# Kernel optimization log

Hardware: AMD Instinct MI355X
Metric: run time of the kernel (lower is better)

## Reference

```python
import jax, jax.numpy as jnp
import numpy as np

N = 50000   # nodes
E = 600000  # edges / hyperedge incidences
D = 128     # node_in_dim
H = 128     # hidden_dim
TAU = 0.5
ALPHA = 0.5
LAM = 0.5

_PARAM_SHAPES = [('Wq0', (1, H)), ('bq0', (H,)), ('W0', (D, H)), ('b0', (H,)),
                 ('Whq0', (1, H)), ('bhq0', (H,)), ('Wh0', (D, H)), ('bh0', (H,)),
                 ('Wf0', (H, H)), ('bf0', (H,)), ('Wfh0', (H, H)), ('bfh0', (H,)),
                 ('aq0', (H,)), ('a0', (H,)), ('ahq0', (H,)), ('ah0', (H,)),
                 ('aq_', (H,)), ('a_', (H,)), ('ahq_', (H,)), ('ah_', (H,)),
                 ('Wlq', (1, H)), ('blq', (H,)), ('Wlf', (D, H)), ('blf', (H,)),
                 ('Wm1', (H, H)), ('bm1', (H,)), ('Wm2', (H, H)), ('bm2', (H,))]


def setup_inputs() -> dict:
    key = jax.random.key(0)
    ks = jax.random.split(key, 8 + len(_PARAM_SHAPES))
    inp = {}
    inp['feats'] = jax.random.normal(ks[0], (N, D), dtype=jnp.float32)
    inp['edge_index'] = jax.random.randint(ks[1], (2, E), 0, N).astype(jnp.int32)
    inp['edge_index_aug'] = jax.random.randint(ks[2], (2, E), 0, N).astype(jnp.int32)
    inp['pos'] = jax.random.randint(ks[3], (100,), 1, N).astype(jnp.int32)
    inp['q'] = 0
    for i, (nm, sh) in enumerate(_PARAM_SHAPES):
        inp[nm] = jax.random.normal(ks[4 + i], sh, dtype=jnp.float32) * 0.05
    return inp


def _forward(feats, Wq0, bq0, W0, b0, Whq0, bhq0, Wh0, bh0, Wf0, bf0, Wfh0, bfh0,
             aq0, a0, ahq0, ah0, aq_, a_, ahq_, ah_, Wlq, blq, Wlf, blf,
             Wm1, bm1, Wm2, bm2, edge_index, edge_index_aug, q, pos):
    # ---- GCNConv (PyG default: add self-loops + symmetric normalization) ----
    sl = jnp.arange(N, dtype=edge_index.dtype)
    src = jnp.concatenate([edge_index[0], sl])
    dst = jnp.concatenate([edge_index[1], sl])
    deg = jax.ops.segment_sum(jnp.ones(src.shape[0], jnp.float32), dst, num_segments=N)
    dinv = jax.lax.rsqrt(deg)  # deg >= 1 thanks to self-loops
    enorm = dinv[src] * dinv[dst]

    def gcn(x, W, b):
        xw = x @ W
        return jax.ops.segment_sum(xw[src] * enorm[:, None], dst, num_segments=N) + b

    # ---- HypergraphConv (PyG, no attention): X' = D^-1 H B^-1 H^T X W ----
    node = edge_index_aug[0]
    he = edge_index_aug[1]
    Be = jax.ops.segment_sum(jnp.ones((E,), jnp.float32), he, num_segments=N)
    Dn = jax.ops.segment_sum(jnp.ones((E,), jnp.float32), node, num_segments=N)
    Binv = jnp.where(Be > 0, 1.0 / Be, 0.0)
    Dninv = jnp.where(Dn > 0, 1.0 / Dn, 0.0)

    def hg(x, W, b):
        xw = x @ W
        me = jax.ops.segment_sum(xw[node], he, num_segments=N) * Binv[:, None]
        return jax.ops.segment_sum(me[he], node, num_segments=N) * Dninv[:, None] + b

    # ---- attention-weighted fusion of two views (softmax over 2 logits) ----
    def fuse(a, b, wa, wb):
        att = jax.nn.softmax(jnp.stack([a @ wa, b @ wb], axis=1), axis=1)  # [N,2]
        return att[:, 0:1] * a + att[:, 1:2] * b

    querys = jnp.zeros((N, 1), jnp.float32).at[q].set(1.0)
    hq = jax.nn.relu(gcn(querys, Wq0, bq0))
    h = jax.nn.relu(gcn(feats, W0, b0))
    hf = fuse(hq, h, aq0, a0)
    h_augq = jax.nn.relu(hg(querys, Whq0, bhq0))
    h_aug = jax.nn.relu(hg(feats, Wh0, bh0))
    h_augf = fuse(h_augq, h_aug, ahq0, ah0)
    querys2 = querys @ Wlq + blq
    feats2 = feats @ Wlf + blf
    hf_ = fuse(querys2, feats2, aq_, a_)
    hf = jax.nn.relu(hf + gcn(hf_, Wf0, bf0))
    hfh_ = fuse(querys2, feats2, ahq_, ah_)
    h_augf = jax.nn.relu(h_augf + hg(hfh_, Wfh0, bfh0))

    def mlp(x):
        return jax.nn.relu(x @ Wm1 + bm1) @ Wm2 + bm2

    z = mlp(hf)
    z_aug = mlp(h_augf)

    # ---- Contra loss ----
    def expcos(v, M):
        num = M @ v
        den = jnp.maximum(jnp.linalg.norm(M, axis=1) * jnp.linalg.norm(v), 1e-8)
        return jnp.exp(num / den / TAU)

    sim1 = expcos(z[q], z)
    sim_aug1 = expcos(z_aug[q], z_aug)
    sim2 = expcos(z[q], z_aug)
    sim_aug2 = expcos(z_aug[q], z)
    mask = jnp.zeros((N,), bool).at[pos].set(True).at[q].set(False)
    nmask = jnp.sum(mask).astype(jnp.float32)

    def nlm(s):  # mean over positives of -log(s_i / sum(s))
        r = jnp.log(jnp.sum(s)) - jnp.log(s)
        return jnp.sum(jnp.where(mask, r, 0.0)) / nmask

    loss_intra = 0.5 * (nlm(sim1) + nlm(sim_aug1))
    loss_inter = 0.5 * (nlm(sim2) + nlm(sim_aug2))
    z_unsup = jnp.log(jnp.sum(sim2)) - jnp.log(sim2[q])
    z_aug_unsup = jnp.log(jnp.sum(sim_aug2)) - jnp.log(sim_aug2[q])
    loss_unsup = 0.5 * z_unsup + 0.5 * z_aug_unsup
    return loss_intra + ALPHA * loss_inter + LAM * loss_unsup


def reference(feats, Wq0, bq0, W0, b0, Whq0, bhq0, Wh0, bh0, Wf0, bf0, Wfh0, bfh0,
              aq0, a0, ahq0, ah0, aq_, a_, ahq_, ah_, Wlq, blq, Wlf, blf,
              Wm1, bm1, Wm2, bm2, edge_index, edge_index_aug, q, pos):
    return _forward(feats, Wq0, bq0, W0, b0, Whq0, bhq0, Wh0, bh0, Wf0, bf0, Wfh0, bfh0,
                    aq0, a0, ahq0, ah0, aq_, a_, ahq_, ah_, Wlq, blq, Wlf, blf,
                    Wm1, bm1, Wm2, bm2, edge_index, edge_index_aug, q, pos)
```

## Files before the change

kernel.cpp:

```cpp
#include <hip/hip_runtime.h>

#define NN 50000
#define EE 600000
#define HH 128
#define TAU_INV 2.0f
#define PSZ 6250
#define CAP 48
#define SSTR 64

typedef __attribute__((ext_vector_type(8))) short short8;
typedef __attribute__((ext_vector_type(4))) float f32x4;
typedef __attribute__((ext_vector_type(2))) float floatx2;

__device__ __forceinline__ float wsum64(float v) {
#pragma unroll
  for (int m = 32; m >= 1; m >>= 1) v += __shfl_xor(v, m, 64);
  return v;
}
__device__ __forceinline__ unsigned short f2bf(float f) {
  unsigned u = __builtin_bit_cast(unsigned, f);
  u = u + 0x7FFFu + ((u >> 16) & 1u);
  return (unsigned short)(u >> 16);
}
__device__ __forceinline__ float bf2f(unsigned short h) {
  unsigned u = ((unsigned)h) << 16;
  return __builtin_bit_cast(float, u);
}
__device__ __forceinline__ unsigned char fp8_enc1(float v) {
  int p = __builtin_amdgcn_cvt_pk_fp8_f32(v, v, 0, false);
  return (unsigned char)(p & 0xFF);
}
__device__ __forceinline__ void fp8x8_dec(uint2 v, float* f) {
  floatx2 a = __builtin_amdgcn_cvt_pk_f32_fp8(v.x, false);
  floatx2 b = __builtin_amdgcn_cvt_pk_f32_fp8(v.x, true);
  floatx2 c = __builtin_amdgcn_cvt_pk_f32_fp8(v.y, false);
  floatx2 d = __builtin_amdgcn_cvt_pk_f32_fp8(v.y, true);
  f[0] = a.x; f[1] = a.y; f[2] = b.x; f[3] = b.y;
  f[4] = c.x; f[5] = c.y; f[6] = d.x; f[7] = d.y;
}
__device__ __forceinline__ uint2 fp8x8_enc(const float* f) {
  int w0 = __builtin_amdgcn_cvt_pk_fp8_f32(f[0], f[1], 0, false);
  w0 = __builtin_amdgcn_cvt_pk_fp8_f32(f[2], f[3], w0, true);
  int w1 = __builtin_amdgcn_cvt_pk_fp8_f32(f[4], f[5], 0, false);
  w1 = __builtin_amdgcn_cvt_pk_fp8_f32(f[6], f[7], w1, true);
  return make_uint2((unsigned)w0, (unsigned)w1);
}

#define LDSW 136


__device__ __forceinline__ void fill_body(const int* __restrict__ ei,
                                          const int* __restrict__ ea,
                                          const int* __restrict__ qp, int* __restrict__ cursor,
                                          unsigned short* __restrict__ slotsA,
                                          unsigned short* __restrict__ slotsB,
                                          unsigned short* __restrict__ slotsC,
                                          float* __restrict__ cntq, int blk, int nblk) {
  const int p = blk & 7;
  const int lo = p * PSZ, hi = lo + PSZ;
  const int q = *qp;
  const int stride = (nblk >> 3) * 256;
  for (int e = (blk >> 3) * 256 + threadIdx.x; e < EE; e += stride) {
    int src = ei[e], dst = ei[EE + e];
    if (dst >= lo && dst < hi) {
      int idx = atomicAdd(&cursor[dst], 1);
      if (idx < CAP) slotsA[dst * SSTR + idx] = (unsigned short)src;
    }
    int node = ea[e], he = ea[EE + e];
    if (he >= lo && he < hi) {
      int idx = atomicAdd(&cursor[NN + he], 1);
      if (idx < CAP) slotsB[he * SSTR + idx] = (unsigned short)node;
      if (node == q) atomicAdd(&cntq[he], 1.0f);
    }
    if (node >= lo && node < hi) {
      int idx = atomicAdd(&cursor[2 * NN + node], 1);
      if (idx < CAP) slotsC[node * SSTR + idx] = (unsigned short)he;
    }
  }
}

__device__ __forceinline__ void pack_body(const float* __restrict__ W0,
                                          const float* __restrict__ Wh0,
                                          const float* __restrict__ Wlf,
                                          const float* __restrict__ Wf0,
                                          const float* __restrict__ Wfh0,
                                          const float* __restrict__ Wm1,
                                          const float* __restrict__ Wm2,
                                          unsigned short* __restrict__ out, int blk) {
  int tid = blk * 256 + threadIdx.x;
  if (tid >= 7 * 2048) return;
  int mat = tid >> 11, r = tid & 2047;
  int s = r >> 9, c = (r >> 6) & 7, lane = r & 63;
  const float* W = (mat == 0) ? W0 : (mat == 1) ? Wh0 : (mat == 2) ? Wlf
                 : (mat == 3) ? Wf0 : (mat == 4) ? Wfh0 : (mat == 5) ? Wm1 : Wm2;
  int k0 = 32 * s + (lane >> 4) * 8;
  int n = 16 * c + (lane & 15);
  unsigned short* o = out + (size_t)tid * 8;
#pragma unroll
  for (int j = 0; j < 8; ++j) o[j] = f2bf(W[(k0 + j) * 128 + n]);
}

__device__ __forceinline__ void derive_body(const int* __restrict__ cursor,
                                            float* __restrict__ dinv, float* __restrict__ Binv,
                                            float* __restrict__ Dninv,
                                            const int* __restrict__ pos,
                                            const int* __restrict__ qp,
                                            int* __restrict__ maskI, int blk) {
  int i = blk * 256 + threadIdx.x;
  if (i < NN) {
    dinv[i] = rsqrtf((float)(cursor[i] + 1));
    int b = cursor[NN + i];
    Binv[i] = (b > 0) ? 1.0f / (float)b : 0.0f;
    int d = cursor[2 * NN + i];
    Dninv[i] = (d > 0) ? 1.0f / (float)d : 0.0f;
  }
  if (blk == 0) {
    int t = threadIdx.x;
    if (t < 100) maskI[pos[t]] = 1;
    __syncthreads();
    if (t == 0) maskI[*qp] = 0;
  }
}

__device__ __forceinline__ void shq_body(const int* __restrict__ ei, const int* __restrict__ ea,
                                         const int* __restrict__ qp,
                                         const int* __restrict__ cursor,
                                         const float* __restrict__ cntq,
                                         float* __restrict__ s_hq, float* __restrict__ s_hgq,
                                         int blk) {
  int e = blk * 256 + threadIdx.x;
  if (e >= EE) return;
  int q = *qp;
  int src = ei[e];
  if (src == q) {
    int dst = ei[EE + e];
    float dq = rsqrtf((float)(cursor[q] + 1));
    atomicAdd(&s_hq[dst], dq * rsqrtf((float)(cursor[dst] + 1)));
  }
  int he = ea[EE + e];
  float cq = cntq[he];
  if (cq != 0.0f) {
    int node = ea[e];
    atomicAdd(&s_hgq[node], cq / (float)cursor[NN + he]);
  }
  if (e == 0) atomicAdd(&s_hq[q], 1.0f / (float)(cursor[q] + 1));
}

template <bool BIAS, int OM>
__device__ __forceinline__ void gemm_core_rt(const unsigned short* As, const short8* Wp,
                                             const float* bias, void* outv, int r0, int nrows,
                                             int tid, int relu) {
  const int wave = tid >> 6, lane = tid & 63;
  const int quad = lane >> 4, l15 = lane & 15;
  const int rw = r0 + wave * 16;
  f32x4 acc[8];
#pragma unroll
  for (int c = 0; c < 8; ++c) acc[c] = (f32x4){0.f, 0.f, 0.f, 0.f};
#pragma unroll
  for (int s = 0; s < 4; ++s) {
    short8 a = *(const short8*)&As[(wave * 16 + l15) * LDSW + s * 32 + quad * 8];
#pragma unroll
    for (int c = 0; c < 8; ++c) {
      short8 b = Wp[(s * 8 + c) * 64 + lane];
      acc[c] = __builtin_amdgcn_mfma_f32_16x16x32_bf16(a, b, acc[c], 0, 0, 0);
    }
  }
#pragma unroll
  for (int c = 0; c < 8; ++c) {
    int col = c * 16 + l15;
    float bv = BIAS ? bias[col] : 0.f;
#pragma unroll
    for (int r = 0; r < 4; ++r) {
      int grow = rw + quad * 4 + r;
      if (grow < nrows) {
        float v = acc[c][r] + bv;
        if (relu) v = fmaxf(v, 0.f);
        if (OM == 2)
          ((unsigned char*)outv)[(size_t)grow * 256 + col] = fp8_enc1(v);
        else
          ((unsigned short*)outv)[(size_t)grow * 128 + col] = f2bf(v);
      }
    }
  }
}

__device__ __forceinline__ void stage_bf16(const unsigned short* A, unsigned short* As,
                                           int r0, int nrows, int tid) {
#pragma unroll
  for (int t = 0; t < 4; ++t) {
    int v = t * 256 + tid;
    int row = v >> 4, cc = v & 15;
    int gr = r0 + row;
    uint4 val = make_uint4(0, 0, 0, 0);
    if (gr < nrows) val = ((const uint4*)A)[(size_t)gr * 16 + cc];
    *(uint4*)&As[row * LDSW + cc * 8] = val;
  }
}

__device__ __forceinline__ void gemm3_body(unsigned short* As, const float* __restrict__ A,
                                           const short8* __restrict__ Wp,
                                           const float* __restrict__ bias2,
                                           unsigned char* __restrict__ p1,
                                           unsigned char* __restrict__ p2,
                                           unsigned short* __restrict__ out2, int nrows,
                                           int blk) {
  const int tid = threadIdx.x;
  const int r0 = blk * 64;
#pragma unroll
  for (int t = 0; t < 8; ++t) {
    int v = t * 256 + tid;
    int row = v >> 5, c4 = v & 31;
    int gr = r0 + row;
    float4 val = make_float4(0.f, 0.f, 0.f, 0.f);
    if (gr < nrows) val = ((const float4*)A)[(size_t)gr * 32 + c4];
    ushort4 o;
    o.x = f2bf(val.x); o.y = f2bf(val.y); o.z = f2bf(val.z); o.w = f2bf(val.w);
    *(ushort4*)&As[row * LDSW + c4 * 4] = o;
  }
  __syncthreads();
  const int wave = tid >> 6, lane = tid & 63;
  const int quad = lane >> 4, l15 = lane & 15;
  const int rw = r0 + wave * 16;
  f32x4 acc[3][8];
#pragma unroll
  for (int m = 0; m < 3; ++m)
#pragma unroll
    for (int c = 0; c < 8; ++c) acc[m][c] = (f32x4){0.f, 0.f, 0.f, 0.f};
#pragma unroll
  for (int s = 0; s < 4; ++s) {
    short8 a = *(const short8*)&As[(wave * 16 + l15) * LDSW + s * 32 + quad * 8];
#pragma unroll
    for (int m = 0; m < 3; ++m)
#pragma unroll
      for (int c = 0; c < 8; ++c) {
        short8 b = Wp[(size_t)m * 2048 + (s * 8 + c) * 64 + lane];
        acc[m][c] = __builtin_amdgcn_mfma_f32_16x16x32_bf16(a, b, acc[m][c], 0, 0, 0);
      }
  }
#pragma unroll
  for (int c = 0; c < 8; ++c) {
    int col = c * 16 + l15;
    float bv = bias2[col];
#pragma unroll
    for (int r = 0; r < 4; ++r) {
      int grow = rw + quad * 4 + r;
      if (grow < nrows) {
        p1[(size_t)grow * 256 + col] = fp8_enc1(acc[0][c][r]);
        p2[(size_t)grow * 256 + col] = fp8_enc1(acc[1][c][r]);
        out2[(size_t)grow * 128 + col] = f2bf(acc[2][c][r] + bv);
      }
    }
  }
}

template <int MODE, bool OUTFP8>
__device__ __forceinline__ void gpair_body(const uint2* __restrict__ xp,
                                           unsigned short* __restrict__ y1,
                                           unsigned short* __restrict__ y2,
                                           uint2* __restrict__ yp,
                                           const int* __restrict__ cnt,
                                           const unsigned short* __restrict__ slots,
                                           const float* __restrict__ wv, int blk) {
  int node = blk * 8 + (threadIdx.x >> 5);
  if (node >= NN) return;
  int l = threadIdx.x & 31;
  int st = node * SSTR;
  int n = min(cnt[node], CAP);
  float acc[8];
#pragma unroll
  for (int i = 0; i < 8; ++i) acc[i] = 0.f;
  int p = 0;
  for (; p + 4 <= n; p += 4) {
    ushort4 s4 = *(const ushort4*)&slots[st + p];
    uint2 v0 = xp[(size_t)s4.x * 32 + l];
    uint2 v1 = xp[(size_t)s4.y * 32 + l];
    uint2 v2 = xp[(size_t)s4.z * 32 + l];
    uint2 v3 = xp[(size_t)s4.w * 32 + l];
    float f[8];
    if (MODE == 0) {
      float w0 = wv[s4.x], w1 = wv[s4.y], w2 = wv[s4.z], w3 = wv[s4.w];
      fp8x8_dec(v0, f);
#pragma unroll
      for (int i = 0; i < 8; ++i) acc[i] = fmaf(w0, f[i], acc[i]);
      fp8x8_dec(v1, f);
#pragma unroll
      for (int i = 0; i < 8; ++i) acc[i] = fmaf(w1, f[i], acc[i]);
      fp8x8_dec(v2, f);
#pragma unroll
      for (int i = 0; i < 8; ++i) acc[i] = fmaf(w2, f[i], acc[i]);
      fp8x8_dec(v3, f);
#pragma unroll
      for (int i = 0; i < 8; ++i) acc[i] = fmaf(w3, f[i], acc[i]);
    } else {
      fp8x8_dec(v0, f);
#pragma unroll
      for (int i = 0; i < 8; ++i) acc[i] += f[i];
      fp8x8_dec(v1, f);
#pragma unroll
      for (int i = 0; i < 8; ++i) acc[i] += f[i];
      fp8x8_dec(v2, f);
#pragma unroll
      for (int i = 0; i < 8; ++i) acc[i] += f[i];
      fp8x8_dec(v3, f);
#pragma unroll
      for (int i = 0; i < 8; ++i) acc[i] += f[i];
    }
  }
  for (; p < n; ++p) {
    int s = slots[st + p];
    uint2 v = xp[(size_t)s * 32 + l];
    float f[8];
    fp8x8_dec(v, f);
    if (MODE == 0) {
      float w = wv[s];
#pragma unroll
      for (int i = 0; i < 8; ++i) acc[i] = fmaf(w, f[i], acc[i]);
    } else {
#pragma unroll
      for (int i = 0; i < 8; ++i) acc[i] += f[i];
    }
  }
  float sc = wv[node];
  if (MODE == 0) {
    uint2 v = xp[(size_t)node * 32 + l];
    float f[8];
    fp8x8_dec(v, f);
#pragma unroll
    for (int i = 0; i < 8; ++i) acc[i] = sc * fmaf(sc, f[i], acc[i]);
  } else {
#pragma unroll
    for (int i = 0; i < 8; ++i) acc[i] *= sc;
  }
  if (OUTFP8) {
    yp[(size_t)node * 32 + l] = fp8x8_enc(acc);
  } else {
    unsigned short* y = (l < 16) ? y1 : y2;
    int cg = l & 15;
    uint4 o;
    o.x = ((unsigned)f2bf(acc[1]) << 16) | f2bf(acc[0]);
    o.y = ((unsigned)f2bf(acc[3]) << 16) | f2bf(acc[2]);
    o.z = ((unsigned)f2bf(acc[5]) << 16) | f2bf(acc[4]);
    o.w = ((unsigned)f2bf(acc[7]) << 16) | f2bf(acc[6]);
    *(uint4*)&y[(size_t)node * 128 + cg * 8] = o;
  }
}

__device__ __forceinline__ void fuse_add_body(const unsigned short* __restrict__ g,
                                              const unsigned short* __restrict__ gr,
                                              const float* __restrict__ svec,
                                              const float* __restrict__ dscale,
                                              const float* __restrict__ Wq,
                                              const float* __restrict__ bq,
                                              const float* __restrict__ bm,
                                              const float* __restrict__ aq,
                                              const float* __restrict__ am,
                                              const float* __restrict__ bres,
                                              unsigned short* __restrict__ out, int blk) {
  int row = blk * 4 + (threadIdx.x >> 6);
  if (row >= NN) return;
  int lane = threadIdx.x & 63;
  int c0 = lane, c1 = lane + 64;
  float s = svec[row];
  if (dscale) s *= dscale[row];
  float hq0 = fmaxf(fmaf(s, Wq[c0], bq[c0]), 0.f);
  float hq1 = fmaxf(fmaf(s, Wq[c1], bq[c1]), 0.f);
  float h0 = fmaxf(bf2f(g[(size_t)row * 128 + c0]) + bm[c0], 0.f);
  float h1 = fmaxf(bf2f(g[(size_t)row * 128 + c1]) + bm[c1], 0.f);
  float dq = wsum64(hq0 * aq[c0] + hq1 * aq[c1]);
  float dm = wsum64(h0 * am[c0] + h1 * am[c1]);
  float mx = fmaxf(dq, dm);
  float e0 = expf(dq - mx), e1 = expf(dm - mx);
  float w0 = e0 / (e0 + e1), w1 = 1.f - w0;
  float r0 = fmaxf(w0 * hq0 + w1 * h0 + bf2f(gr[(size_t)row * 128 + c0]) + bres[c0], 0.f);
  float r1 = fmaxf(w0 * hq1 + w1 * h1 + bf2f(gr[(size_t)row * 128 + c1]) + bres[c1], 0.f);
  out[(size_t)row * 128 + c0] = f2bf(r0);
  out[(size_t)row * 128 + c1] = f2bf(r1);
}


__global__ __launch_bounds__(256) void fill_pack_k(
    const int* ei, const int* ea, const int* qp, int* cursor, unsigned short* slotsA,
    unsigned short* slotsB, unsigned short* slotsC, float* cntq, int fb, const float* W0,
    const float* Wh0, const float* Wlf, const float* Wf0, const float* Wfh0, const float* Wm1,
    const float* Wm2, unsigned short* Wpack) {
  int b = blockIdx.x;
  if (b < fb)
    fill_body(ei, ea, qp, cursor, slotsA, slotsB, slotsC, cntq, b, fb);
  else
    pack_body(W0, Wh0, Wlf, Wf0, Wfh0, Wm1, Wm2, Wpack, b - fb);
}

__global__ __launch_bounds__(256) void g3ds_k(
    const float* A, const short8* Wp, const float* bias2, unsigned char* p1, unsigned char* p2,
    unsigned short* out2, int gmb, const int* cursor, float* dinv, float* Binv, float* Dninv,
    const int* pos, const int* qp, int* maskI, const int* ei, const int* ea, const float* cntq,
    float* s_hq, float* s_hgq, int nb) {
  __shared__ unsigned short As[64 * LDSW];
  int b = blockIdx.x;
  if (b < gmb) {
    gemm3_body(As, A, Wp, bias2, p1, p2, out2, NN, b);
    return;
  }
  b -= gmb;
  if (b < nb) {
    derive_body(cursor, dinv, Binv, Dninv, pos, qp, maskI, b);
    return;
  }
  shq_body(ei, ea, qp, cursor, cntq, s_hq, s_hgq, b - nb);
}

__global__ void fuse2_k(const unsigned short* __restrict__ f2, const int* __restrict__ qp,
                        const float* __restrict__ Wlq, const float* __restrict__ blq,
                        const float* __restrict__ aq1, const float* __restrict__ a1,
                        const float* __restrict__ aq2, const float* __restrict__ a2,
                        unsigned short* __restrict__ out1, unsigned short* __restrict__ out2) {
  int row = blockIdx.x * 4 + (threadIdx.x >> 6);
  if (row >= NN) return;
  int lane = threadIdx.x & 63;
  int c0 = lane, c1 = lane + 64;
  int q = *qp;
  float q20 = blq[c0] + ((row == q) ? Wlq[c0] : 0.f);
  float q21 = blq[c1] + ((row == q) ? Wlq[c1] : 0.f);
  float f0 = bf2f(f2[(size_t)row * 128 + c0]);
  float f1 = bf2f(f2[(size_t)row * 128 + c1]);
  float dq1 = wsum64(q20 * aq1[c0] + q21 * aq1[c1]);
  float df1 = wsum64(f0 * a1[c0] + f1 * a1[c1]);
  float dq2 = wsum64(q20 * aq2[c0] + q21 * aq2[c1]);
  float df2 = wsum64(f0 * a2[c0] + f1 * a2[c1]);
  {
    float mx = fmaxf(dq1, df1);
    float e0 = expf(dq1 - mx), e1 = expf(df1 - mx);
    float w0 = e0 / (e0 + e1), w1 = 1.f - w0;
    out1[(size_t)row * 128 + c0] = f2bf(w0 * q20 + w1 * f0);
    out1[(size_t)row * 128 + c1] = f2bf(w0 * q21 + w1 * f1);
  }
  {
    float mx = fmaxf(dq2, df2);
    float e0 = expf(dq2 - mx), e1 = expf(df2 - mx);
    float w0 = e0 / (e0 + e1), w1 = 1.f - w0;
    out2[(size_t)row * 128 + c0] = f2bf(w0 * q20 + w1 * f0);
    out2[(size_t)row * 128 + c1] = f2bf(w0 * q21 + w1 * f1);
  }
}

__global__ __launch_bounds__(256) void gemm2f8_k(const unsigned short* A0,
                                                 const unsigned short* A1, const short8* Wp0,
                                                 const short8* Wp1, unsigned char* o0,
                                                 unsigned char* o1, int nblk) {
  __shared__ unsigned short As[64 * LDSW];
  int b = blockIdx.x;
  const unsigned short* A = A0;
  const short8* Wp = Wp0;
  unsigned char* o = o0;
  if (b >= nblk) {
    b -= nblk; A = A1; Wp = Wp1; o = o1;
  }
  stage_bf16(A, As, b * 64, NN, threadIdx.x);
  __syncthreads();
  gemm_core_rt<false, 2>(As, Wp, nullptr, o, b * 64, NN, threadIdx.x, 0);
}

__global__ void dgather12_k(const uint2* __restrict__ xp1, unsigned short* __restrict__ y1a,
                            unsigned short* __restrict__ y1b, const uint2* __restrict__ xp2,
                            uint2* __restrict__ yp3, const int* __restrict__ cursor,
                            const unsigned short* __restrict__ slotsA,
                            const unsigned short* __restrict__ slotsB,
                            const float* __restrict__ dinv, const float* __restrict__ Binv,
                            int nblk) {
  int b = blockIdx.x;
  if (b < nblk)
    gpair_body<0, false>(xp1, y1a, y1b, nullptr, cursor, slotsA, dinv, b);
  else
    gpair_body<1, true>(xp2, nullptr, nullptr, yp3, cursor + NN, slotsB, Binv, b - nblk);
}

__global__ void g3fa_k(const uint2* xp, unsigned short* y1, unsigned short* y2,
                       const int* cursor, const unsigned short* slotsC, const float* Dninv,
                       int gtb, const unsigned short* g, const unsigned short* gr,
                       const float* svec, const float* Wq, const float* bq, const float* bm,
                       const float* aq, const float* am, const float* bres,
                       unsigned short* out) {
  int b = blockIdx.x;
  if (b < gtb)
    gpair_body<1, false>(xp, y1, y2, nullptr, cursor + 2 * NN, slotsC, Dninv, b);
  else
    fuse_add_body(g, gr, svec, nullptr, Wq, bq, bm, aq, am, bres, out, b - gtb);
}

__global__ __launch_bounds__(256) void fagemm_k(
    const unsigned short* g, const unsigned short* gr, const float* svec, const float* dscale,
    const float* Wq, const float* bq, const float* bm, const float* aq, const float* am,
    const float* bres, unsigned short* out, int rb, const unsigned short* A, const short8* Wp,
    const float* bias, unsigned short* o, int relu) {
  __shared__ unsigned short As[64 * LDSW];
  int b = blockIdx.x;
  if (b < rb) {
    fuse_add_body(g, gr, svec, dscale, Wq, bq, bm, aq, am, bres, out, b);
    return;
  }
  b -= rb;
  stage_bf16(A, As, b * 64, NN, threadIdx.x);
  __syncthreads();
  gemm_core_rt<true, 1>(As, Wp, bias, o, b * 64, NN, threadIdx.x, relu);
}

__global__ __launch_bounds__(256) void gemm2x_k(const unsigned short* A0,
                                                const unsigned short* A1, const short8* Wp0,
                                                const short8* Wp1, const float* b0,
                                                const float* b1, unsigned short* o0,
                                                unsigned short* o1, int nblk, int relu0,
                                                int relu1) {
  __shared__ unsigned short As[64 * LDSW];
  int b = blockIdx.x;
  const unsigned short* A = A0;
  const short8* Wp = Wp0;
  const float* bias = b0;
  unsigned short* o = o0;
  int relu = relu0;
  if (b >= nblk) {
    b -= nblk; A = A1; Wp = Wp1; bias = b1; o = o1; relu = relu1;
  }
  stage_bf16(A, As, b * 64, NN, threadIdx.x);
  __syncthreads();
  gemm_core_rt<true, 1>(As, Wp, bias, o, b * 64, NN, threadIdx.x, relu);
}

__global__ void sim_k(const unsigned short* __restrict__ z,
                      const unsigned short* __restrict__ za, const int* __restrict__ qp,
                      float4* __restrict__ simbuf, float* __restrict__ scal_out) {
  int row = blockIdx.x * 4 + (threadIdx.x >> 6);
  if (row >= NN) return;
  int lane = threadIdx.x & 63;
  int c0 = lane, c1 = lane + 64;
  int q = *qp;
  float zi0 = bf2f(z[(size_t)row * 128 + c0]), zi1 = bf2f(z[(size_t)row * 128 + c1]);
  float zai0 = bf2f(za[(size_t)row * 128 + c0]), zai1 = bf2f(za[(size_t)row * 128 + c1]);
  float zq0 = bf2f(z[(size_t)q * 128 + c0]), zq1 = bf2f(z[(size_t)q * 128 + c1]);
  float zaq0 = bf2f(za[(size_t)q * 128 + c0]), zaq1 = bf2f(za[(size_t)q * 128 + c1]);
  float nzi = wsum64(zi0 * zi0 + zi1 * zi1);
  float nzai = wsum64(zai0 * zai0 + zai1 * zai1);
  float nzq = wsum64(zq0 * zq0 + zq1 * zq1);
  float nzaq = wsum64(zaq0 * zaq0 + zaq1 * zaq1);
  float d1 = wsum64(zi0 * zq0 + zi1 * zq1);
  float d2 = wsum64(zai0 * zaq0 + zai1 * zaq1);
  float d3 = wsum64(zai0 * zq0 + zai1 * zq1);
  float d4 = wsum64(zi0 * zaq0 + zi1 * zaq1);
  if (lane == 0) {
    float ni = sqrtf(nzi), nai = sqrtf(nzai);
    float nq = sqrtf(nzq), naq = sqrtf(nzaq);
    float c1_ = d1 / fmaxf(ni * nq, 1e-8f) * TAU_INV;
    float ca1 = d2 / fmaxf(nai * naq, 1e-8f) * TAU_INV;
    float c2_ = d3 / fmaxf(nai * nq, 1e-8f) * TAU_INV;
    float ca2 = d4 / fmaxf(ni * naq, 1e-8f) * TAU_INV;
    simbuf[row] = make_float4(c1_, ca1, c2_, ca2);
    if (row == q) {
      scal_out[9] = c2_;
      scal_out[10] = ca2;
    }
  }
}

__global__ __launch_bounds__(256) void reduce_sim_k(const float4* __restrict__ simbuf,
                                                    const int* __restrict__ maskI,
                                                    float* __restrict__ scal) {
  float acc[9];
#pragma unroll
  for (int i = 0; i < 9; ++i) acc[i] = 0.f;
  for (int row = blockIdx.x * 256 + threadIdx.x; row < NN; row += gridDim.x * 256) {
    float4 v = simbuf[row];
    acc[0] += expf(v.x);
    acc[1] += expf(v.y);
    acc[2] += expf(v.z);
    acc[3] += expf(v.w);
    if (maskI[row]) {
      acc[4] += v.x; acc[5] += v.y; acc[6] += v.z; acc[7] += v.w;
      acc[8] += 1.0f;
    }
  }
  __shared__ float s[9][4];
  int lane = threadIdx.x & 63, wv = threadIdx.x >> 6;
#pragma unroll
  for (int i = 0; i < 9; ++i) {
    float r = wsum64(acc[i]);
    if (lane == 0) s[i][wv] = r;
  }
  __syncthreads();
  if (threadIdx.x < 9) {
    float r = s[threadIdx.x][0] + s[threadIdx.x][1] + s[threadIdx.x][2] + s[threadIdx.x][3];
    atomicAdd(&scal[threadIdx.x], r);
  }
}

__global__ void final_k(const float* __restrict__ scal, float* __restrict__ out) {
  if (threadIdx.x != 0 || blockIdx.x != 0) return;
  float S1 = scal[0], Sa1 = scal[1], S2 = scal[2], Sa2 = scal[3];
  float L1 = scal[4], La1 = scal[5], L2 = scal[6], La2 = scal[7];
  float NM = scal[8], Q2 = scal[9], Qa2 = scal[10];
  float intra = 0.5f * ((logf(S1) - L1 / NM) + (logf(Sa1) - La1 / NM));
  float inter = 0.5f * ((logf(S2) - L2 / NM) + (logf(Sa2) - La2 / NM));
  float unsup = 0.5f * (logf(S2) - Q2) + 0.5f * (logf(Sa2) - Qa2);
  out[0] = intra + 0.5f * inter + 0.5f * unsup;
}

extern "C" void kernel_launch(void* const* d_in, const int* in_sizes, int n_in,
                              void* d_out, int out_size, void* d_ws, size_t ws_size,
                              hipStream_t stream) {
  const float* feats = (const float*)d_in[0];
  const int* ei = (const int*)d_in[1];
  const int* ea = (const int*)d_in[2];
  const int* pos = (const int*)d_in[3];
  const int* qp = (const int*)d_in[4];
  const float* Wq0 = (const float*)d_in[5];
  const float* bq0 = (const float*)d_in[6];
  const float* W0 = (const float*)d_in[7];
  const float* b0 = (const float*)d_in[8];
  const float* Whq0 = (const float*)d_in[9];
  const float* bhq0 = (const float*)d_in[10];
  const float* Wh0 = (const float*)d_in[11];
  const float* bh0 = (const float*)d_in[12];
  const float* Wf0 = (const float*)d_in[13];
  const float* bf0 = (const float*)d_in[14];
  const float* Wfh0 = (const float*)d_in[15];
  const float* bfh0 = (const float*)d_in[16];
  const float* aq0 = (const float*)d_in[17];
  const float* a0 = (const float*)d_in[18];
  const float* ahq0 = (const float*)d_in[19];
  const float* ah0 = (const float*)d_in[20];
  const float* aq_ = (const float*)d_in[21];
  const float* a_ = (const float*)d_in[22];
  const float* ahq_ = (const float*)d_in[23];
  const float* ah_ = (const float*)d_in[24];
  const float* Wlq = (const float*)d_in[25];
  const float* blq = (const float*)d_in[26];
  const float* Wlf = (const float*)d_in[27];
  const float* blf = (const float*)d_in[28];
  const float* Wm1 = (const float*)d_in[29];
  const float* bm1 = (const float*)d_in[30];
  const float* Wm2 = (const float*)d_in[31];
  const float* bm2 = (const float*)d_in[32];

  char* ws = (char*)d_ws;
  size_t off = 0;
  auto take = [&](size_t bytes) -> void* {
    void* p = ws + off;
    off = (off + bytes + 255) & ~(size_t)255;
    return p;
  };
  int* cursor3 = (int*)take(3 * NN * 4);
  int* maskI = (int*)take(NN * 4);
  float* s_hq = (float*)take(NN * 4);
  float* cntq = (float*)take(NN * 4);
  float* s_hgq = (float*)take(NN * 4);
  float* scal = (float*)take(64 * 4);
  size_t zero_end = off;
  unsigned short* slotsA = (unsigned short*)take((size_t)NN * SSTR * 2);
  unsigned short* slotsB = (unsigned short*)take((size_t)NN * SSTR * 2);
  unsigned short* slotsC = (unsigned short*)take((size_t)NN * SSTR * 2);
  float* dinv = (float*)take(NN * 4);
  float* Binv = (float*)take(NN * 4);
  float* Dninv = (float*)take(NN * 4);
  float4* simbuf = (float4*)take((size_t)NN * 16);
  unsigned short* Wpack = (unsigned short*)take((size_t)7 * 16384 * 2);
  const size_t BFSZ = (size_t)NN * HH * 2;
  unsigned short* B0 = (unsigned short*)take(BFSZ);
  unsigned short* B1 = (unsigned short*)take(BFSZ);
  unsigned short* B2 = (unsigned short*)take(BFSZ);
  unsigned short* B3 = (unsigned short*)take(BFSZ);
  unsigned short* B4 = (unsigned short*)take(BFSZ);
  unsigned short* B5 = (unsigned short*)take(BFSZ);
  unsigned short* B6 = (unsigned short*)take(BFSZ);
  unsigned char* P1 = (unsigned char*)take((size_t)NN * 256);
  unsigned char* P2 = (unsigned char*)take((size_t)NN * 256);
  unsigned char* P3 = (unsigned char*)take((size_t)NN * 256);

  const int NB = (NN + 255) / 256;
  const int EB = (EE + 255) / 256;
  const int GMB = (NN + 63) / 64;
  const int GTB = (NN + 7) / 8;
  const int RB = (NN + 3) / 4;
  const int FB = 4096;
  const int PB = 56;
  const short8* Wp = (const short8*)Wpack;

  hipMemsetAsync(d_ws, 0, zero_end, stream);
  fill_pack_k<<<FB + PB, 256, 0, stream>>>(ei, ea, qp, cursor3, slotsA, slotsB, slotsC, cntq,
                                           FB, W0, Wh0, Wlf, Wf0, Wfh0, Wm1, Wm2, Wpack);
  g3ds_k<<<GMB + NB + EB, 256, 0, stream>>>(feats, Wp, blf, P1, P2, B6, GMB, cursor3, dinv,
                                            Binv, Dninv, pos, qp, maskI, ei, ea, cntq, s_hq,
                                            s_hgq, NB);
  fuse2_k<<<RB, 256, 0, stream>>>(B6, qp, Wlq, blq, aq_, a_, ahq_, ah_, B3, B4);
  gemm2f8_k<<<2 * GMB, 256, 0, stream>>>(B3, B4, Wp + (size_t)3 * 2048, Wp + (size_t)4 * 2048,
                                         P1 + 128, P2 + 128, GMB);
  dgather12_k<<<2 * GTB, 256, 0, stream>>>((const uint2*)P1, B0, B1, (const uint2*)P2,
                                           (uint2*)P3, cursor3, slotsA, slotsB, dinv, Binv,
                                           GTB);
  g3fa_k<<<GTB + RB, 256, 0, stream>>>((const uint2*)P3, B2, B5, cursor3, slotsC, Dninv, GTB,
                                       B0, B1, s_hq, Wq0, bq0, b0, aq0, a0, bf0, B3);
  fagemm_k<<<RB + GMB, 256, 0, stream>>>(B2, B5, s_hgq, Dninv, Whq0, bhq0, bh0, ahq0, ah0,
                                         bfh0, B4, RB, B3, Wp + (size_t)5 * 2048, bm1, B0, 1);
  gemm2x_k<<<2 * GMB, 256, 0, stream>>>(B4, B0, Wp + (size_t)5 * 2048, Wp + (size_t)6 * 2048,
                                        bm1, bm2, B1, B2, GMB, 1, 0);
  gemm2x_k<<<GMB, 256, 0, stream>>>(B1, B1, Wp + (size_t)6 * 2048, Wp + (size_t)6 * 2048, bm2,
                                    bm2, B5, B5, GMB, 0, 0);
  sim_k<<<RB, 256, 0, stream>>>(B2, B5, qp, simbuf, scal);
  reduce_sim_k<<<64, 256, 0, stream>>>(simbuf, maskI, scal);
  final_k<<<1, 64, 0, stream>>>(scal, (float*)d_out);
}
```

Baseline: 477.2 us.

## Regroup early kernels to overlap fill with GEMM, unroll gather by eight

Weight packing moves into its own small kernel so the first GEMM can share a launch with the edge-fill pass. The degree derivation, query-scalar and fuse2 steps merge into a single launch, which removes one kernel boundary. The gather loop now loads eight slot indices with one 16-byte read and issues eight independent row loads, and the slot stride is reduced to match the capacity. Costs are higher register pressure in the gather and a mixed-work launch whose GEMM blocks compete with atomic-heavy fill blocks.

```diff
diff --git a/kernel.cpp b/kernel.cpp
--- a/kernel.cpp
+++ b/kernel.cpp
@@ -6,7 +6,7 @@
 #define TAU_INV 2.0f
 #define PSZ 6250
 #define CAP 48
-#define SSTR 64
+#define SSTR 48
 
 typedef __attribute__((ext_vector_type(8))) short short8;
 typedef __attribute__((ext_vector_type(4))) float f32x4;
@@ -79,27 +79,6 @@
   }
 }
 
-__device__ __forceinline__ void pack_body(const float* __restrict__ W0,
-                                          const float* __restrict__ Wh0,
-                                          const float* __restrict__ Wlf,
-                                          const float* __restrict__ Wf0,
-                                          const float* __restrict__ Wfh0,
-                                          const float* __restrict__ Wm1,
-                                          const float* __restrict__ Wm2,
-                                          unsigned short* __restrict__ out, int blk) {
-  int tid = blk * 256 + threadIdx.x;
-  if (tid >= 7 * 2048) return;
-  int mat = tid >> 11, r = tid & 2047;
-  int s = r >> 9, c = (r >> 6) & 7, lane = r & 63;
-  const float* W = (mat == 0) ? W0 : (mat == 1) ? Wh0 : (mat == 2) ? Wlf
-                 : (mat == 3) ? Wf0 : (mat == 4) ? Wfh0 : (mat == 5) ? Wm1 : Wm2;
-  int k0 = 32 * s + (lane >> 4) * 8;
-  int n = 16 * c + (lane & 15);
-  unsigned short* o = out + (size_t)tid * 8;
-#pragma unroll
-  for (int j = 0; j < 8; ++j) o[j] = f2bf(W[(k0 + j) * 128 + n]);
-}
-
 __device__ __forceinline__ void derive_body(const int* __restrict__ cursor,
                                             float* __restrict__ dinv, float* __restrict__ Binv,
                                             float* __restrict__ Dninv,
@@ -270,15 +249,22 @@
 #pragma unroll
   for (int i = 0; i < 8; ++i) acc[i] = 0.f;
   int p = 0;
-  for (; p + 4 <= n; p += 4) {
-    ushort4 s4 = *(const ushort4*)&slots[st + p];
-    uint2 v0 = xp[(size_t)s4.x * 32 + l];
-    uint2 v1 = xp[(size_t)s4.y * 32 + l];
-    uint2 v2 = xp[(size_t)s4.z * 32 + l];
-    uint2 v3 = xp[(size_t)s4.w * 32 + l];
+  for (; p + 8 <= n; p += 8) {
+    uint4 sl = *(const uint4*)&slots[st + p];
+    int i0 = sl.x & 0xFFFF, i1 = sl.x >> 16, i2 = sl.y & 0xFFFF, i3 = sl.y >> 16;
+    int i4 = sl.z & 0xFFFF, i5 = sl.z >> 16, i6 = sl.w & 0xFFFF, i7 = sl.w >> 16;
+    uint2 v0 = xp[(size_t)i0 * 32 + l];
+    uint2 v1 = xp[(size_t)i1 * 32 + l];
+    uint2 v2 = xp[(size_t)i2 * 32 + l];
+    uint2 v3 = xp[(size_t)i3 * 32 + l];
+    uint2 v4 = xp[(size_t)i4 * 32 + l];
+    uint2 v5 = xp[(size_t)i5 * 32 + l];
+    uint2 v6 = xp[(size_t)i6 * 32 + l];
+    uint2 v7 = xp[(size_t)i7 * 32 + l];
     float f[8];
     if (MODE == 0) {
-      float w0 = wv[s4.x], w1 = wv[s4.y], w2 = wv[s4.z], w3 = wv[s4.w];
+      float w0 = wv[i0], w1 = wv[i1], w2 = wv[i2], w3 = wv[i3];
+      float w4 = wv[i4], w5 = wv[i5], w6 = wv[i6], w7 = wv[i7];
       fp8x8_dec(v0, f);
 #pragma unroll
       for (int i = 0; i < 8; ++i) acc[i] = fmaf(w0, f[i], acc[i]);
@@ -291,6 +277,18 @@
       fp8x8_dec(v3, f);
 #pragma unroll
       for (int i = 0; i < 8; ++i) acc[i] = fmaf(w3, f[i], acc[i]);
+      fp8x8_dec(v4, f);
+#pragma unroll
+      for (int i = 0; i < 8; ++i) acc[i] = fmaf(w4, f[i], acc[i]);
+      fp8x8_dec(v5, f);
+#pragma unroll
+      for (int i = 0; i < 8; ++i) acc[i] = fmaf(w5, f[i], acc[i]);
+      fp8x8_dec(v6, f);
+#pragma unroll
+      for (int i = 0; i < 8; ++i) acc[i] = fmaf(w6, f[i], acc[i]);
+      fp8x8_dec(v7, f);
+#pragma unroll
+      for (int i = 0; i < 8; ++i) acc[i] = fmaf(w7, f[i], acc[i]);
     } else {
       fp8x8_dec(v0, f);
 #pragma unroll
@@ -302,6 +300,18 @@
 #pragma unroll
       for (int i = 0; i < 8; ++i) acc[i] += f[i];
       fp8x8_dec(v3, f);
+#pragma unroll
+      for (int i = 0; i < 8; ++i) acc[i] += f[i];
+      fp8x8_dec(v4, f);
+#pragma unroll
+      for (int i = 0; i < 8; ++i) acc[i] += f[i];
+      fp8x8_dec(v5, f);
+#pragma unroll
+      for (int i = 0; i < 8; ++i) acc[i] += f[i];
+      fp8x8_dec(v6, f);
+#pragma unroll
+      for (int i = 0; i < 8; ++i) acc[i] += f[i];
+      fp8x8_dec(v7, f);
 #pragma unroll
       for (int i = 0; i < 8; ++i) acc[i] += f[i];
     }
@@ -377,44 +387,17 @@
   out[(size_t)row * 128 + c1] = f2bf(r1);
 }
 
-
-__global__ __launch_bounds__(256) void fill_pack_k(
-    const int* ei, const int* ea, const int* qp, int* cursor, unsigned short* slotsA,
-    unsigned short* slotsB, unsigned short* slotsC, float* cntq, int fb, const float* W0,
-    const float* Wh0, const float* Wlf, const float* Wf0, const float* Wfh0, const float* Wm1,
-    const float* Wm2, unsigned short* Wpack) {
-  int b = blockIdx.x;
-  if (b < fb)
-    fill_body(ei, ea, qp, cursor, slotsA, slotsB, slotsC, cntq, b, fb);
-  else
-    pack_body(W0, Wh0, Wlf, Wf0, Wfh0, Wm1, Wm2, Wpack, b - fb);
-}
-
-__global__ __launch_bounds__(256) void g3ds_k(
-    const float* A, const short8* Wp, const float* bias2, unsigned char* p1, unsigned char* p2,
-    unsigned short* out2, int gmb, const int* cursor, float* dinv, float* Binv, float* Dninv,
-    const int* pos, const int* qp, int* maskI, const int* ei, const int* ea, const float* cntq,
-    float* s_hq, float* s_hgq, int nb) {
-  __shared__ unsigned short As[64 * LDSW];
-  int b = blockIdx.x;
-  if (b < gmb) {
-    gemm3_body(As, A, Wp, bias2, p1, p2, out2, NN, b);
-    return;
-  }
-  b -= gmb;
-  if (b < nb) {
-    derive_body(cursor, dinv, Binv, Dninv, pos, qp, maskI, b);
-    return;
-  }
-  shq_body(ei, ea, qp, cursor, cntq, s_hq, s_hgq, b - nb);
-}
-
-__global__ void fuse2_k(const unsigned short* __restrict__ f2, const int* __restrict__ qp,
-                        const float* __restrict__ Wlq, const float* __restrict__ blq,
-                        const float* __restrict__ aq1, const float* __restrict__ a1,
-                        const float* __restrict__ aq2, const float* __restrict__ a2,
-                        unsigned short* __restrict__ out1, unsigned short* __restrict__ out2) {
-  int row = blockIdx.x * 4 + (threadIdx.x >> 6);
+__device__ __forceinline__ void fuse2_body(const unsigned short* __restrict__ f2,
+                                           const int* __restrict__ qp,
+                                           const float* __restrict__ Wlq,
+                                           const float* __restrict__ blq,
+                                           const float* __restrict__ aq1,
+                                           const float* __restrict__ a1,
+                                           const float* __restrict__ aq2,
+                                           const float* __restrict__ a2,
+                                           unsigned short* __restrict__ out1,
+                                           unsigned short* __restrict__ out2, int blk) {
+  int row = blk * 4 + (threadIdx.x >> 6);
   if (row >= NN) return;
   int lane = threadIdx.x & 63;
   int c0 = lane, c1 = lane + 64;
@@ -441,6 +424,56 @@
     out2[(size_t)row * 128 + c0] = f2bf(w0 * q20 + w1 * f0);
     out2[(size_t)row * 128 + c1] = f2bf(w0 * q21 + w1 * f1);
   }
+}
+
+
+__global__ void pack_k(const float* __restrict__ W0, const float* __restrict__ Wh0,
+                       const float* __restrict__ Wlf, const float* __restrict__ Wf0,
+                       const float* __restrict__ Wfh0, const float* __restrict__ Wm1,
+                       const float* __restrict__ Wm2, unsigned short* __restrict__ out) {
+  int tid = blockIdx.x * 256 + threadIdx.x;
+  if (tid >= 7 * 2048) return;
+  int mat = tid >> 11, r = tid & 2047;
+  int s = r >> 9, c = (r >> 6) & 7, lane = r & 63;
+  const float* W = (mat == 0) ? W0 : (mat == 1) ? Wh0 : (mat == 2) ? Wlf
+                 : (mat == 3) ? Wf0 : (mat == 4) ? Wfh0 : (mat == 5) ? Wm1 : Wm2;
+  int k0 = 32 * s + (lane >> 4) * 8;
+  int n = 16 * c + (lane & 15);
+  unsigned short* o = out + (size_t)tid * 8;
+#pragma unroll
+  for (int j = 0; j < 8; ++j) o[j] = f2bf(W[(k0 + j) * 128 + n]);
+}
+
+__global__ __launch_bounds__(256) void g3fill_k(
+    const float* A, const short8* Wp, const float* bias2, unsigned char* p1, unsigned char* p2,
+    unsigned short* out2, int gmb, const int* ei, const int* ea, const int* qp, int* cursor,
+    unsigned short* slotsA, unsigned short* slotsB, unsigned short* slotsC, float* cntq,
+    int fb) {
+  __shared__ unsigned short As[64 * LDSW];
+  int b = blockIdx.x;
+  if (b < gmb)
+    gemm3_body(As, A, Wp, bias2, p1, p2, out2, NN, b);
+  else
+    fill_body(ei, ea, qp, cursor, slotsA, slotsB, slotsC, cntq, b - gmb, fb);
+}
+
+__global__ void dsf_k(const int* ei, const int* ea, const int* qp, const int* cursor,
+                      const float* cntq, float* s_hq, float* s_hgq, int eb, float* dinv,
+                      float* Binv, float* Dninv, const int* pos, int* maskI, int nb,
+                      const unsigned short* f2, const float* Wlq, const float* blq,
+                      const float* aq1, const float* a1, const float* aq2, const float* a2,
+                      unsigned short* out1, unsigned short* out2) {
+  int b = blockIdx.x;
+  if (b < eb) {
+    shq_body(ei, ea, qp, cursor, cntq, s_hq, s_hgq, b);
+    return;
+  }
+  b -= eb;
+  if (b < nb) {
+    derive_body(cursor, dinv, Binv, Dninv, pos, qp, maskI, b);
+    return;
+  }
+  fuse2_body(f2, qp, Wlq, blq, aq1, a1, aq2, a2, out1, out2, b - nb);
 }
 
 __global__ __launch_bounds__(256) void gemm2f8_k(const unsigned short* A0,
@@ -679,16 +712,15 @@
   const int GTB = (NN + 7) / 8;
   const int RB = (NN + 3) / 4;
   const int FB = 4096;
-  const int PB = 56;
   const short8* Wp = (const short8*)Wpack;
 
   hipMemsetAsync(d_ws, 0, zero_end, stream);
-  fill_pack_k<<<FB + PB, 256, 0, stream>>>(ei, ea, qp, cursor3, slotsA, slotsB, slotsC, cntq,
-                                           FB, W0, Wh0, Wlf, Wf0, Wfh0, Wm1, Wm2, Wpack);
-  g3ds_k<<<GMB + NB + EB, 256, 0, stream>>>(feats, Wp, blf, P1, P2, B6, GMB, cursor3, dinv,
-                                            Binv, Dninv, pos, qp, maskI, ei, ea, cntq, s_hq,
-                                            s_hgq, NB);
-  fuse2_k<<<RB, 256, 0, stream>>>(B6, qp, Wlq, blq, aq_, a_, ahq_, ah_, B3, B4);
+  pack_k<<<56, 256, 0, stream>>>(W0, Wh0, Wlf, Wf0, Wfh0, Wm1, Wm2, Wpack);
+  g3fill_k<<<GMB + FB, 256, 0, stream>>>(feats, Wp, blf, P1, P2, B6, GMB, ei, ea, qp, cursor3,
+                                         slotsA, slotsB, slotsC, cntq, FB);
+  dsf_k<<<EB + NB + RB, 256, 0, stream>>>(ei, ea, qp, cursor3, cntq, s_hq, s_hgq, EB, dinv,
+                                          Binv, Dninv, pos, maskI, NB, B6, Wlq, blq, aq_, a_,
+                                          ahq_, ah_, B3, B4);
   gemm2f8_k<<<2 * GMB, 256, 0, stream>>>(B3, B4, Wp + (size_t)3 * 2048, Wp + (size_t)4 * 2048,
                                          P1 + 128, P2 + 128, GMB);
   dgather12_k<<<2 * GTB, 256, 0, stream>>>((const uint2*)P1, B0, B1, (const uint2*)P2,
```

Measured after the change: 515.1 us. +8.0%, slower.
